# Kernel optimization log

Measured on AMD Instinct MI355X. Metric: run time of the kernel, lower is better.

The kernel has to match this reference:

```python
import jax, jax.numpy as jnp
import numpy as np

B, S, V, H, E, T, MAXLEN = 16, 100, 30000, 512, 300, 50, 50
NEG = -1e6


def setup_inputs() -> dict:
    key = jax.random.key(0)
    ks = jax.random.split(key, 12)
    D = 3 * H + E
    d = {}
    d["encoder_outputs"] = jax.random.normal(ks[0], (B, S, H), jnp.float32)
    d["temp_outputs"] = jax.random.normal(ks[1], (B, T, H), jnp.float32)
    d["z"] = jax.random.normal(ks[2], (B, H), jnp.float32)
    d["embedding"] = jax.random.normal(ks[3], (V, E), jnp.float32) * 0.02
    d["gru_w_ih"] = jax.random.normal(ks[4], (3 * H, D), jnp.float32) * (1.0 / np.sqrt(H))
    d["gru_w_hh"] = jax.random.normal(ks[5], (3 * H, H), jnp.float32) * (1.0 / np.sqrt(H))
    d["gru_b_ih"] = jnp.zeros((3 * H,), jnp.float32)
    d["gru_b_hh"] = jnp.zeros((3 * H,), jnp.float32)
    d["attn_w"] = jax.random.normal(ks[6], (H, H), jnp.float32) * (1.0 / np.sqrt(H))
    d["attn_b"] = jnp.zeros((H,), jnp.float32)
    d["copy_w"] = jax.random.normal(ks[7], (H, H), jnp.float32) * (1.0 / np.sqrt(H))
    d["copy_b"] = jnp.zeros((H,), jnp.float32)
    d["out_w"] = jax.random.normal(ks[8], (V, 2 * H), jnp.float32) * (1.0 / np.sqrt(2 * H))
    d["out_b"] = jnp.zeros((V,), jnp.float32)
    d["templates"] = jax.random.randint(ks[9], (B, T), 0, V, jnp.int32)
    d["inputs"] = jax.random.randint(ks[10], (B, S), 0, V, jnp.int32)
    return d


def _forward(encoder_outputs, temp_outputs, z, embedding,
             gru_w_ih, gru_w_hh, gru_b_ih, gru_b_hh,
             attn_w, attn_b, copy_w, copy_b, out_w, out_b,
             templates, inputs):
    # one-hot over extended vocab (vocab + source positions), as in to_one_hot
    one_hot = jax.nn.one_hot(inputs, V + S, dtype=jnp.float32)      # (B,S,V+S)
    missing = (one_hot.sum(axis=1) == 0).at[:, 0].set(True)          # (B,V+S)
    rows = jnp.arange(B)
    cols = jnp.arange(S)

    def gru_cell(x, h):  # torch nn.GRU single step
        gi = x @ gru_w_ih.T + gru_b_ih
        gh = h @ gru_w_hh.T + gru_b_hh
        ir, iz, inn = jnp.split(gi, 3, axis=-1)
        hr, hz, hn = jnp.split(gh, 3, axis=-1)
        r = jax.nn.sigmoid(ir + hr)
        zg = jax.nn.sigmoid(iz + hz)
        n = jnp.tanh(inn + r * hn)
        return (1.0 - zg) * n + zg * h

    def decode_step(prev_idx, pre_hidden, t_hidden, sel_read):
        idx = jnp.where(prev_idx > V, 3, prev_idx)                   # OOV -> <UNK>=3
        emb = embedding[idx]                                         # (B,E)
        x = jnp.concatenate([pre_hidden, t_hidden, sel_read, emb], axis=-1)
        hidden = gru_cell(x, pre_hidden)                             # (B,H); output==hidden for 1 step
        th = hidden @ attn_w.T + attn_b
        aw = jax.nn.softmax(jnp.einsum('bsh,bh->bs', encoder_outputs, th), axis=-1)
        context = jnp.einsum('bs,bsh->bh', aw, encoder_outputs)
        gen = jnp.concatenate([context, hidden], axis=-1) @ out_w.T + out_b
        gen = gen.at[:, 0].set(NEG)
        th2 = hidden @ copy_w.T + copy_b
        css = jnp.einsum('bsh,bh->bs', encoder_outputs, th2)         # copy_score_seq (B,S)
        copy_scores = jnp.where(missing, NEG, jnp.einsum('bs,bsv->bv', css, one_hot))
        probs = jax.nn.softmax(jnp.concatenate([gen, copy_scores], axis=-1), axis=-1)
        final = jnp.pad(probs[:, :V], ((0, 0), (0, S))) + probs[:, V:]  # (B,V+S)
        sampled = jnp.argmax(jnp.log(final + 1e-10), axis=-1).astype(jnp.int32)
        pos = one_hot[rows[:, None], cols[None, :], sampled[:, None]]   # (B,S)
        sel = pos * css
        sel = sel / jnp.maximum(jnp.sum(jnp.abs(sel), axis=-1, keepdims=True), 1e-12)
        new_sel = jnp.einsum('bs,bsh->bh', sel, encoder_outputs)
        return sampled, final, hidden, new_sel

    beg = jnp.ones((B,), jnp.int32)  # vocab['<BEG>'] == 1
    carry0 = dict(hidden=z, pre_hidden=z, sampled=beg, pre_sampled=beg, eos=beg,
                  pre_seg=templates[:, 0], index=jnp.zeros((B,), jnp.int32),
                  c_len=jnp.zeros((B,), jnp.int32), sel=jnp.zeros((B, H), jnp.float32))

    def body(c, _):
        # eos bookkeeping: keep last non-<EOS>(6) sample
        eos_new = jnp.where(c['pre_sampled'] == 6, c['eos'], c['pre_sampled'])
        # mask_tf=True template advance
        flag = (c['pre_seg'] != 5) | (c['pre_sampled'] == 6) | (c['c_len'] > 20)
        index = c['index'] + flag.astype(jnp.int32)
        c_len = c['c_len'] + (~flag).astype(jnp.int32)
        seg = templates[rows, index]
        t_hidden = temp_outputs[rows, index]                         # (B,H)
        sampled = jnp.where(flag, seg, c['sampled'])                 # masked_scatter of seg
        pre_sampled = sampled
        # rows emitting 5/6 keep their old pre_hidden
        keep = (sampled == 5) | (sampled == 6)
        pre_hidden = jnp.where(keep[:, None], c['pre_hidden'], c['hidden'])
        sampled = jnp.where(sampled == 6, eos_new, sampled)
        new_sampled, output, hidden, sel = decode_step(sampled, pre_hidden, t_hidden, c['sel'])
        new_c = dict(hidden=hidden, pre_hidden=pre_hidden, sampled=new_sampled,
                     pre_sampled=pre_sampled, eos=eos_new, pre_seg=seg,
                     index=index, c_len=c_len, sel=sel)
        return new_c, (output, pre_sampled)

    _, (outs, idxs) = jax.lax.scan(body, carry0, None, length=MAXLEN - 1)
    sos = jnp.zeros((B, V + S), jnp.float32).at[:, 1].set(1.0)
    decoder_outputs = jnp.concatenate([sos[:, None, :], jnp.swapaxes(outs, 0, 1)], axis=1)
    sampled_idxs = jnp.concatenate([beg[:, None], idxs.T], axis=1)
    return decoder_outputs, sampled_idxs


def reference(encoder_outputs, temp_outputs, z, embedding,
              gru_w_ih, gru_w_hh, gru_b_ih, gru_b_hh,
              attn_w, attn_b, copy_w, copy_b, out_w, out_b,
              templates, inputs):
    return _forward(encoder_outputs, temp_outputs, z, embedding,
                    gru_w_ih, gru_w_hh, gru_b_ih, gru_b_hh,
                    attn_w, attn_b, copy_w, copy_b, out_w, out_b,
                    templates, inputs)
```

## Files before the change

kernel.cpp:

```cpp
#include <hip/hip_runtime.h>
#include <math.h>

#define NEGV (-1000000.0f)

constexpr size_t WS_WT_OUT = 0;
constexpr size_t WS_WT_IH  = 30720000;
constexpr size_t WS_WT_HH  = 33540096;
constexpr size_t WS_WT_AT  = 34326528;
constexpr size_t WS_WT_CP  = 34588672;
constexpr size_t WS_XG     = 34850816;
constexpr size_t WS_X2     = 34880192;
constexpr size_t WS_PGI    = 34896576;
constexpr size_t WS_PGH    = 35093184;
constexpr size_t WS_PTH    = 35289792;
constexpr size_t WS_PTH2   = 35322560;
constexpr size_t WS_HID    = 35355328;
constexpr size_t WS_PREH   = 35363520;
constexpr size_t WS_CSS    = 35371712;
constexpr size_t WS_CVAL   = 35373312;
constexpr size_t WS_COPYZ  = 35374912;
constexpr size_t WS_MCUR   = 35374928;
constexpr size_t WS_ZPART  = 35374944;
constexpr size_t WS_ZTOT   = 35382480;
constexpr size_t WS_INTS   = 35383264;
constexpr size_t IP_CTOK = 0;
constexpr size_t IP_EOS  = 1600;
constexpr size_t IP_PS   = 1616;
constexpr size_t IP_SEG  = 1632;
constexpr size_t IP_IDX  = 1648;
constexpr size_t IP_CLEN = 1664;

constexpr size_t OUT_BSTRIDE = 1505000;
constexpr size_t IDX_OFF = 24080000;

__global__ void ktrans(const float* __restrict__ src, float* __restrict__ dst, int R, int C) {
  __shared__ float tile[32][33];
  const int t = threadIdx.x;
  const int lx = t & 31, ly = t >> 5;
  const int r0 = blockIdx.x * 32, c0 = blockIdx.y * 32;
  #pragma unroll
  for (int i = 0; i < 4; ++i) {
    int r = r0 + ly + i * 8, c = c0 + lx;
    if (r < R && c < C) tile[ly + i * 8][lx] = src[(size_t)r * C + c];
  }
  __syncthreads();
  #pragma unroll
  for (int i = 0; i < 4; ++i) {
    int c = c0 + ly + i * 8, r = r0 + lx;
    if (r < R && c < C) dst[(size_t)c * R + r] = tile[lx][ly + i * 8];
  }
}

__global__ void kinit(float* ws, float* out, const float* __restrict__ z,
                      const int* __restrict__ templates, const float* __restrict__ temp_outputs,
                      const float* __restrict__ embedding) {
  const int bid = blockIdx.x, t = threadIdx.x;
  if (bid < 1882) {
    int e = bid * 256 + t;
    if (e < 16 * 30100) {
      int b = e / 30100, v = e % 30100;
      out[(size_t)b * OUT_BSTRIDE + v] = (v == 1) ? 1.0f : 0.0f;
    }
    return;
  }
  const int b = bid - 1882;
  const int tpl0 = templates[b * 50];
  const int ps = 1, eos = 1;
  const int eos_new = (ps == 6) ? eos : ps;
  const bool flag = (tpl0 != 5) || (ps == 6);
  const int index = flag ? 1 : 0;
  const int clen = flag ? 0 : 1;
  const int seg = templates[b * 50 + index];
  const int sampled2 = flag ? seg : 1;
  const int sampled3 = (sampled2 == 6) ? eos_new : sampled2;
  const int idx_emb = (sampled3 > 30000) ? 3 : (sampled3 > 29999 ? 29999 : sampled3);
  float* xg = ws + WS_XG;
  for (int d = t; d < 512; d += 256) {
    float zv = z[b * 512 + d];
    xg[d * 16 + b] = zv;
    ws[WS_PREH + b * 512 + d] = zv;
    xg[(512 + d) * 16 + b] = temp_outputs[(size_t)(b * 50 + index) * 512 + d];
    xg[(1024 + d) * 16 + b] = 0.0f;
  }
  for (int d = t; d < 300; d += 256)
    xg[(1536 + d) * 16 + b] = embedding[(size_t)idx_emb * 300 + d];
  if (t == 0) {
    int* ip = (int*)ws;
    ip[WS_INTS + IP_EOS + b] = eos_new;
    ip[WS_INTS + IP_PS + b] = sampled2;
    ip[WS_INTS + IP_SEG + b] = seg;
    ip[WS_INTS + IP_IDX + b] = index;
    ip[WS_INTS + IP_CLEN + b] = clen;
    out[IDX_OFF + b * 50 + 0] = 1.0f;
    out[IDX_OFF + b * 50 + 1] = (float)sampled2;
  }
}

__global__ void k1(float* ws) {
  const int bid = blockIdx.x, t = threadIdx.x;
  const int lane = t & 63;
  const int bq = __builtin_amdgcn_readfirstlane(t >> 6);
  const int b0 = bq * 4;
  const float* xg = ws + WS_XG;
  const bool is_gi = bid < 192;
  const int sub = is_gi ? bid : bid - 192;
  const int jc = sub >> 3, ks = sub & 7;
  const int j = jc * 64 + lane;
  const float* W;
  int d0, d1;
  float* pout;
  if (is_gi) {
    W = ws + WS_WT_IH; d0 = ks * 230; d1 = d0 + 230; if (d1 > 1836) d1 = 1836;
    pout = ws + WS_PGI;
  } else {
    W = ws + WS_WT_HH; d0 = ks * 64; d1 = d0 + 64;
    pout = ws + WS_PGH;
  }
  float a0 = 0.f, a1 = 0.f, a2 = 0.f, a3 = 0.f;
  const float* xrow = xg + b0;
  for (int d = d0; d < d1; ++d) {
    float w = W[(size_t)d * 1536 + j];
    float4 xv = *(const float4*)(xrow + d * 16);
    a0 += w * xv.x; a1 += w * xv.y; a2 += w * xv.z; a3 += w * xv.w;
  }
  *(float4*)(pout + ((size_t)ks * 1536 + j) * 16 + b0) = make_float4(a0, a1, a2, a3);
}

__global__ void k1b(float* ws, const float* __restrict__ bih, const float* __restrict__ bhh) {
  const int bid = blockIdx.x;
  const int b = bid >> 1;
  const int j = (bid & 1) * 256 + threadIdx.x;
  float gir = 0.f, giz = 0.f, gin = 0.f, ghr = 0.f, ghz = 0.f, ghn = 0.f;
  #pragma unroll
  for (int ks = 0; ks < 8; ++ks) {
    const float* pg = ws + WS_PGI + (size_t)ks * 1536 * 16;
    gir += pg[j * 16 + b]; giz += pg[(512 + j) * 16 + b]; gin += pg[(1024 + j) * 16 + b];
    const float* ph = ws + WS_PGH + (size_t)ks * 1536 * 16;
    ghr += ph[j * 16 + b]; ghz += ph[(512 + j) * 16 + b]; ghn += ph[(1024 + j) * 16 + b];
  }
  gir += bih[j]; giz += bih[512 + j]; gin += bih[1024 + j];
  ghr += bhh[j]; ghz += bhh[512 + j]; ghn += bhh[1024 + j];
  float r  = 1.f / (1.f + expf(-(gir + ghr)));
  float zg = 1.f / (1.f + expf(-(giz + ghz)));
  float n  = tanhf(gin + r * ghn);
  float h  = ws[WS_PREH + b * 512 + j];
  float hn = (1.f - zg) * n + zg * h;
  ws[WS_HID + b * 512 + j] = hn;
  ws[WS_X2 + (size_t)(512 + j) * 16 + b] = hn;
}

__global__ void k2(float* ws) {
  const int bid = blockIdx.x, t = threadIdx.x;
  const int lane = t & 63;
  const int bq = __builtin_amdgcn_readfirstlane(t >> 6);
  const int b0 = bq * 4;
  const bool is_th = bid < 32;
  const int sub = is_th ? bid : bid - 32;
  const int jc = sub >> 2, ks = sub & 3;
  const int j = jc * 64 + lane;
  const float* W = ws + (is_th ? WS_WT_AT : WS_WT_CP);
  float* pout = ws + (is_th ? WS_PTH : WS_PTH2);
  const float* xh = ws + WS_X2 + 512 * 16 + b0;
  const int d0 = ks * 128, d1 = d0 + 128;
  float a0 = 0.f, a1 = 0.f, a2 = 0.f, a3 = 0.f;
  for (int d = d0; d < d1; ++d) {
    float w = W[(size_t)d * 512 + j];
    float4 xv = *(const float4*)(xh + d * 16);
    a0 += w * xv.x; a1 += w * xv.y; a2 += w * xv.z; a3 += w * xv.w;
  }
  *(float4*)(pout + ((size_t)ks * 512 + j) * 16 + b0) = make_float4(a0, a1, a2, a3);
}

__global__ void k2b(float* ws, const float* __restrict__ attn_b, const float* __restrict__ copy_b,
                    const float* __restrict__ enc, const int* __restrict__ inputs) {
  const int b = blockIdx.x, t = threadIdx.x;
  __shared__ float th_s[512], th2_s[512];
  __shared__ float sc_s[128], css_s[128], e_s[128];
  __shared__ float aw_s[100];
  __shared__ int   tok_s[100];
  __shared__ float gs_s[100];
  __shared__ int   valid_s[100];
  __shared__ float red[256];

  for (int j = t; j < 512; j += 256) {
    float s1 = attn_b[j], s2 = copy_b[j];
    #pragma unroll
    for (int ks = 0; ks < 4; ++ks) {
      s1 += ws[WS_PTH  + ((size_t)ks * 512 + j) * 16 + b];
      s2 += ws[WS_PTH2 + ((size_t)ks * 512 + j) * 16 + b];
    }
    th_s[j] = s1; th2_s[j] = s2;
  }
  if (t < 128) { sc_s[t] = -1e30f; css_s[t] = 0.f; }
  if (t < 100) tok_s[t] = inputs[b * 100 + t];
  __syncthreads();

  const int w = t >> 6, lane = t & 63;
  for (int s = w; s < 100; s += 4) {
    const float* er = enc + (size_t)(b * 100 + s) * 512;
    float p1 = 0.f, p2 = 0.f;
    #pragma unroll
    for (int i = 0; i < 8; ++i) {
      float e = er[lane + 64 * i];
      p1 += e * th_s[lane + 64 * i];
      p2 += e * th2_s[lane + 64 * i];
    }
    for (int off = 32; off > 0; off >>= 1) { p1 += __shfl_down(p1, off); p2 += __shfl_down(p2, off); }
    if (lane == 0) { sc_s[s] = p1; css_s[s] = p2; ws[WS_CSS + b * 100 + s] = p2; }
  }
  __syncthreads();

  if (t < 64) {
    float m = fmaxf(sc_s[t], sc_s[t + 64]);
    for (int off = 32; off > 0; off >>= 1) m = fmaxf(m, __shfl_down(m, off));
    if (t == 0) red[0] = m;
  }
  __syncthreads();
  const float m = red[0];
  if (t < 128) e_s[t] = (t < 100) ? expf(sc_s[t] - m) : 0.f;
  __syncthreads();
  if (t < 64) {
    float ss = e_s[t] + e_s[t + 64];
    for (int off = 32; off > 0; off >>= 1) ss += __shfl_down(ss, off);
    if (t == 0) red[1] = ss;
  }
  __syncthreads();
  const float inv = 1.f / red[1];
  if (t < 100) aw_s[t] = e_s[t] * inv;
  __syncthreads();

  for (int d = t; d < 512; d += 256) {
    float c = 0.f;
    for (int s = 0; s < 100; ++s) c += aw_s[s] * enc[(size_t)(b * 100 + s) * 512 + d];
    ws[WS_X2 + (size_t)d * 16 + b] = c;
  }

  if (t < 100) {
    int tok = tok_s[t]; float gs = 0.f; bool first = true;
    for (int s2 = 0; s2 < 100; ++s2) {
      if (tok_s[s2] == tok) { gs += css_s[s2]; if (s2 < t) first = false; }
    }
    gs_s[t] = gs; valid_s[t] = (first && tok != 0) ? 1 : 0;
  }
  __syncthreads();
  if (t < 64) {
    float v1 = (t < 100 && valid_s[t]) ? gs_s[t] : -1e30f;
    float v2 = ((t + 64) < 100 && valid_s[t + 64]) ? gs_s[t + 64] : -1e30f;
    float m2 = fmaxf(v1, v2);
    for (int off = 32; off > 0; off >>= 1) m2 = fmaxf(m2, __shfl_down(m2, off));
    if (t == 0) red[2] = fmaxf(m2, 0.f);
  }
  __syncthreads();
  const float M = red[2];
  float cv = 0.f;
  if (t < 100) {
    cv = valid_s[t] ? expf(gs_s[t] - M) : 0.f;
    ws[WS_CVAL + b * 100 + t] = cv;
    ((int*)ws)[WS_INTS + IP_CTOK + b * 100 + t] = tok_s[t];
  }
  red[t] = cv;
  __syncthreads();
  for (int off = 128; off > 0; off >>= 1) { if (t < off) red[t] += red[t + off]; __syncthreads(); }
  if (t == 0) { ws[WS_COPYZ + b] = red[0]; ws[WS_MCUR + b] = M; }
}

__global__ void k3(float* ws, const float* __restrict__ outb, float* out, int step) {
  const int bid = blockIdx.x, t = threadIdx.x;
  const int lane = t & 63;
  const int bq = __builtin_amdgcn_readfirstlane(t >> 6);
  const int b0 = bq * 4;
  const int v = bid * 64 + lane;
  const float* Wt = ws + WS_WT_OUT;
  const float* xrow = ws + WS_X2 + b0;
  float p0 = 0.f, p1 = 0.f, p2 = 0.f, p3 = 0.f;
  if (v < 30000) {
    float a0 = 0.f, a1 = 0.f, a2 = 0.f, a3 = 0.f;
    #pragma unroll 8
    for (int k = 0; k < 1024; ++k) {
      float wv = Wt[(size_t)k * 30000 + v];
      float4 xv = *(const float4*)(xrow + k * 16);
      a0 += wv * xv.x; a1 += wv * xv.y; a2 += wv * xv.z; a3 += wv * xv.w;
    }
    if (v != 0) {
      const float bb = outb[v];
      p0 = expf(a0 + bb - ws[WS_MCUR + b0 + 0]);
      p1 = expf(a1 + bb - ws[WS_MCUR + b0 + 1]);
      p2 = expf(a2 + bb - ws[WS_MCUR + b0 + 2]);
      p3 = expf(a3 + bb - ws[WS_MCUR + b0 + 3]);
    }
  }
  if (v < 30100) {
    const size_t rb = (size_t)(step + 1) * 30100 + v;
    out[(size_t)(b0 + 0) * OUT_BSTRIDE + rb] = p0;
    out[(size_t)(b0 + 1) * OUT_BSTRIDE + rb] = p1;
    out[(size_t)(b0 + 2) * OUT_BSTRIDE + rb] = p2;
    out[(size_t)(b0 + 3) * OUT_BSTRIDE + rb] = p3;
  }
  float s0 = p0, s1 = p1, s2 = p2, s3 = p3;
  for (int off = 32; off > 0; off >>= 1) {
    s0 += __shfl_down(s0, off); s1 += __shfl_down(s1, off);
    s2 += __shfl_down(s2, off); s3 += __shfl_down(s3, off);
  }
  __shared__ float wp[4][4];
  if (lane == 0) { wp[bq][0] = s0; wp[bq][1] = s1; wp[bq][2] = s2; wp[bq][3] = s3; }
  __syncthreads();
  if (t < 16) ws[WS_ZPART + (size_t)bid * 16 + t] = wp[t >> 2][t & 3];
}

__global__ void k4b(float* ws, float* out, const float* __restrict__ enc, const int* __restrict__ inputs,
                    const int* __restrict__ templates, const float* __restrict__ temp_outputs,
                    const float* __restrict__ embedding, int step) {
  const int b = blockIdx.x, t = threadIdx.x;
  int* ip = (int*)ws;
  const size_t row = (size_t)b * OUT_BSTRIDE + (size_t)(step + 1) * 30100;
  __shared__ float red[256];
  __shared__ int redi[256];
  __shared__ float selv_s[100];
  __shared__ float sh_inv;

  float zp = 0.f;
  for (int i = t; i < 471; i += 256) zp += ws[WS_ZPART + (size_t)i * 16 + b];
  red[t] = zp; __syncthreads();
  for (int off = 128; off > 0; off >>= 1) { if (t < off) red[t] += red[t + off]; __syncthreads(); }
  if (t == 0) ws[WS_ZTOT + step * 16 + b] = red[0] + ws[WS_COPYZ + b];
  __syncthreads();

  if (t < 100) {
    float cv = ws[WS_CVAL + b * 100 + t];
    if (cv > 0.f) {
      int tok = ip[WS_INTS + IP_CTOK + b * 100 + t];
      out[row + tok] += cv;
    }
  }
  __syncthreads();
  if (step >= 48) return;

  float bp = -1.f; int bv = 0;
  for (int v = t; v < 30100; v += 256) {
    float p = out[row + v];
    if (p > bp) { bp = p; bv = v; }
  }
  red[t] = bp; redi[t] = bv; __syncthreads();
  for (int off = 128; off > 0; off >>= 1) {
    if (t < off) {
      float po = red[t + off]; int vo = redi[t + off];
      if (po > red[t] || (po == red[t] && vo < redi[t])) { red[t] = po; redi[t] = vo; }
    }
    __syncthreads();
  }
  const int samp = redi[0];
  __syncthreads();

  float sv = 0.f;
  if (t < 100) {
    sv = (inputs[b * 100 + t] == samp) ? ws[WS_CSS + b * 100 + t] : 0.f;
    selv_s[t] = sv;
  }
  red[t] = (t < 100) ? fabsf(sv) : 0.f;
  __syncthreads();
  for (int off = 128; off > 0; off >>= 1) { if (t < off) red[t] += red[t + off]; __syncthreads(); }
  if (t == 0) sh_inv = 1.f / fmaxf(red[0], 1e-12f);
  __syncthreads();
  if (t < 100) selv_s[t] = selv_s[t] * sh_inv;
  __syncthreads();

  const int ps = ip[WS_INTS + IP_PS + b], eos = ip[WS_INTS + IP_EOS + b];
  const int preseg = ip[WS_INTS + IP_SEG + b], index = ip[WS_INTS + IP_IDX + b];
  const int clen = ip[WS_INTS + IP_CLEN + b];
  const int eos_new = (ps == 6) ? eos : ps;
  const bool flag = (preseg != 5) || (ps == 6) || (clen > 20);
  const int index_n = index + (flag ? 1 : 0);
  const int clen_n = clen + (flag ? 0 : 1);
  const int seg = templates[b * 50 + index_n];
  const int sampled2 = flag ? seg : samp;
  const bool keep = (sampled2 == 5) || (sampled2 == 6);
  const int sampled3 = (sampled2 == 6) ? eos_new : sampled2;
  const int idx_emb = (sampled3 > 30000) ? 3 : (sampled3 > 29999 ? 29999 : sampled3);

  float* xg = ws + WS_XG;
  for (int d = t; d < 512; d += 256) {
    float phv = keep ? ws[WS_PREH + b * 512 + d] : ws[WS_HID + b * 512 + d];
    ws[WS_PREH + b * 512 + d] = phv;
    xg[d * 16 + b] = phv;
    xg[(512 + d) * 16 + b] = temp_outputs[(size_t)(b * 50 + index_n) * 512 + d];
    float sr = 0.f;
    for (int s = 0; s < 100; ++s) sr += selv_s[s] * enc[(size_t)(b * 100 + s) * 512 + d];
    xg[(1024 + d) * 16 + b] = sr;
  }
  for (int d = t; d < 300; d += 256)
    xg[(1536 + d) * 16 + b] = embedding[(size_t)idx_emb * 300 + d];
  if (t == 0) {
    ip[WS_INTS + IP_PS + b] = sampled2;
    ip[WS_INTS + IP_EOS + b] = eos_new;
    ip[WS_INTS + IP_SEG + b] = seg;
    ip[WS_INTS + IP_IDX + b] = index_n;
    ip[WS_INTS + IP_CLEN + b] = clen_n;
    out[IDX_OFF + b * 50 + step + 2] = (float)sampled2;
  }
}

__global__ void knorm(const float* __restrict__ ws, float* out) {
  const int e = blockIdx.x * 256 + threadIdx.x;
  if (e >= 23598400) return;
  const int b = e / 1474900;
  const int r2 = e - b * 1474900;
  const int r = r2 / 30100;
  const int v = r2 - r * 30100;
  out[(size_t)b * OUT_BSTRIDE + (size_t)(r + 1) * 30100 + v] /= ws[WS_ZTOT + r * 16 + b];
}

extern "C" void kernel_launch(void* const* d_in, const int* in_sizes, int n_in,
                              void* d_out, int out_size, void* d_ws, size_t ws_size,
                              hipStream_t stream) {
  const float* enc       = (const float*)d_in[0];
  const float* temp_out  = (const float*)d_in[1];
  const float* z         = (const float*)d_in[2];
  const float* embedding = (const float*)d_in[3];
  const float* gru_w_ih  = (const float*)d_in[4];
  const float* gru_w_hh  = (const float*)d_in[5];
  const float* gru_b_ih  = (const float*)d_in[6];
  const float* gru_b_hh  = (const float*)d_in[7];
  const float* attn_w    = (const float*)d_in[8];
  const float* attn_b    = (const float*)d_in[9];
  const float* copy_w    = (const float*)d_in[10];
  const float* copy_b    = (const float*)d_in[11];
  const float* out_w     = (const float*)d_in[12];
  const float* out_b     = (const float*)d_in[13];
  const int*   templates = (const int*)d_in[14];
  const int*   inputs    = (const int*)d_in[15];
  float* out = (float*)d_out;
  float* ws  = (float*)d_ws;

  ktrans<<<dim3(938, 32), 256, 0, stream>>>(out_w, ws + WS_WT_OUT, 30000, 1024);
  ktrans<<<dim3(48, 58), 256, 0, stream>>>(gru_w_ih, ws + WS_WT_IH, 1536, 1836);
  ktrans<<<dim3(48, 16), 256, 0, stream>>>(gru_w_hh, ws + WS_WT_HH, 1536, 512);
  ktrans<<<dim3(16, 16), 256, 0, stream>>>(attn_w, ws + WS_WT_AT, 512, 512);
  ktrans<<<dim3(16, 16), 256, 0, stream>>>(copy_w, ws + WS_WT_CP, 512, 512);

  kinit<<<1898, 256, 0, stream>>>(ws, out, z, templates, temp_out, embedding);

  for (int step = 0; step < 49; ++step) {
    k1<<<384, 256, 0, stream>>>(ws);
    k1b<<<32, 256, 0, stream>>>(ws, gru_b_ih, gru_b_hh);
    k2<<<64, 256, 0, stream>>>(ws);
    k2b<<<16, 256, 0, stream>>>(ws, attn_b, copy_b, enc, inputs);
    k3<<<471, 256, 0, stream>>>(ws, out_b, out, step);
    k4b<<<16, 256, 0, stream>>>(ws, out, enc, inputs, templates, temp_out, embedding, step);
  }

  knorm<<<92182, 256, 0, stream>>>(ws, out);
}
```

Measured before the change: 11.62 ms.

## Store output projection weights in bf16 and fuse argmax into logits kernel

The transposed 30000x1024 output weight matrix is stored as bf16 instead of fp32, halving the bytes k3 streams on each of the 49 decode steps. k3 also computes a per-block argmax of its logits and writes it to workspace. k4b then reduces these partial maxima and checks only the copy-token positions, instead of rescanning the full 30100-wide output row. bf16 weights add rounding error that could flip greedy argmax picks relative to the fp32 reference.

```diff
diff --git a/kernel.cpp b/kernel.cpp
--- a/kernel.cpp
+++ b/kernel.cpp
@@ -4,34 +4,42 @@
 #define NEGV (-1000000.0f)
 
 constexpr size_t WS_WT_OUT = 0;
-constexpr size_t WS_WT_IH  = 30720000;
-constexpr size_t WS_WT_HH  = 33540096;
-constexpr size_t WS_WT_AT  = 34326528;
-constexpr size_t WS_WT_CP  = 34588672;
-constexpr size_t WS_XG     = 34850816;
-constexpr size_t WS_X2     = 34880192;
-constexpr size_t WS_PGI    = 34896576;
-constexpr size_t WS_PGH    = 35093184;
-constexpr size_t WS_PTH    = 35289792;
-constexpr size_t WS_PTH2   = 35322560;
-constexpr size_t WS_HID    = 35355328;
-constexpr size_t WS_PREH   = 35363520;
-constexpr size_t WS_CSS    = 35371712;
-constexpr size_t WS_CVAL   = 35373312;
-constexpr size_t WS_COPYZ  = 35374912;
-constexpr size_t WS_MCUR   = 35374928;
-constexpr size_t WS_ZPART  = 35374944;
-constexpr size_t WS_ZTOT   = 35382480;
-constexpr size_t WS_INTS   = 35383264;
+constexpr size_t WS_WT_IH  = 15360000;
+constexpr size_t WS_WT_HH  = 18180096;
+constexpr size_t WS_WT_AT  = 18966528;
+constexpr size_t WS_WT_CP  = 19228672;
+constexpr size_t WS_XG     = 19490816;
+constexpr size_t WS_X2     = 19520192;
+constexpr size_t WS_PGI    = 19536576;
+constexpr size_t WS_PGH    = 19733184;
+constexpr size_t WS_PTH    = 19929792;
+constexpr size_t WS_PTH2   = 19962560;
+constexpr size_t WS_HID    = 19995328;
+constexpr size_t WS_PREH   = 20003520;
+constexpr size_t WS_CSS    = 20011712;
+constexpr size_t WS_CVAL   = 20013312;
+constexpr size_t WS_COPYZ  = 20014912;
+constexpr size_t WS_MCUR   = 20014928;
+constexpr size_t WS_ZPART  = 20014944;
+constexpr size_t WS_ZTOT   = 20022480;
+constexpr size_t WS_AMV    = 20023264;
+constexpr size_t WS_INTS   = 20030800;
 constexpr size_t IP_CTOK = 0;
 constexpr size_t IP_EOS  = 1600;
 constexpr size_t IP_PS   = 1616;
 constexpr size_t IP_SEG  = 1632;
 constexpr size_t IP_IDX  = 1648;
 constexpr size_t IP_CLEN = 1664;
+constexpr size_t IP_AMI  = 1680;
 
 constexpr size_t OUT_BSTRIDE = 1505000;
 constexpr size_t IDX_OFF = 24080000;
+
+__device__ inline unsigned short f2bf(float x) {
+  unsigned u = __float_as_uint(x);
+  unsigned r = (u + 0x7fffu + ((u >> 16) & 1u)) >> 16;
+  return (unsigned short)r;
+}
 
 __global__ void ktrans(const float* __restrict__ src, float* __restrict__ dst, int R, int C) {
   __shared__ float tile[32][33];
@@ -48,6 +56,24 @@
   for (int i = 0; i < 4; ++i) {
     int c = c0 + ly + i * 8, r = r0 + lx;
     if (r < R && c < C) dst[(size_t)c * R + r] = tile[lx][ly + i * 8];
+  }
+}
+
+__global__ void ktransb(const float* __restrict__ src, unsigned short* __restrict__ dst, int R, int C) {
+  __shared__ float tile[32][33];
+  const int t = threadIdx.x;
+  const int lx = t & 31, ly = t >> 5;
+  const int r0 = blockIdx.x * 32, c0 = blockIdx.y * 32;
+  #pragma unroll
+  for (int i = 0; i < 4; ++i) {
+    int r = r0 + ly + i * 8, c = c0 + lx;
+    if (r < R && c < C) tile[ly + i * 8][lx] = src[(size_t)r * C + c];
+  }
+  __syncthreads();
+  #pragma unroll
+  for (int i = 0; i < 4; ++i) {
+    int c = c0 + ly + i * 8, r = r0 + lx;
+    if (r < R && c < C) dst[(size_t)c * R + r] = f2bf(tile[lx][ly + i * 8]);
   }
 }
 
@@ -96,7 +122,7 @@
   }
 }
 
-__global__ void k1(float* ws) {
+__global__ __launch_bounds__(256) void k1(float* ws) {
   const int bid = blockIdx.x, t = threadIdx.x;
   const int lane = t & 63;
   const int bq = __builtin_amdgcn_readfirstlane(t >> 6);
@@ -126,7 +152,7 @@
   *(float4*)(pout + ((size_t)ks * 1536 + j) * 16 + b0) = make_float4(a0, a1, a2, a3);
 }
 
-__global__ void k1b(float* ws, const float* __restrict__ bih, const float* __restrict__ bhh) {
+__global__ __launch_bounds__(256) void k1b(float* ws, const float* __restrict__ bih, const float* __restrict__ bhh) {
   const int bid = blockIdx.x;
   const int b = bid >> 1;
   const int j = (bid & 1) * 256 + threadIdx.x;
@@ -149,7 +175,7 @@
   ws[WS_X2 + (size_t)(512 + j) * 16 + b] = hn;
 }
 
-__global__ void k2(float* ws) {
+__global__ __launch_bounds__(256) void k2(float* ws) {
   const int bid = blockIdx.x, t = threadIdx.x;
   const int lane = t & 63;
   const int bq = __builtin_amdgcn_readfirstlane(t >> 6);
@@ -171,7 +197,7 @@
   *(float4*)(pout + ((size_t)ks * 512 + j) * 16 + b0) = make_float4(a0, a1, a2, a3);
 }
 
-__global__ void k2b(float* ws, const float* __restrict__ attn_b, const float* __restrict__ copy_b,
+__global__ __launch_bounds__(256) void k2b(float* ws, const float* __restrict__ attn_b, const float* __restrict__ copy_b,
                     const float* __restrict__ enc, const int* __restrict__ inputs) {
   const int b = blockIdx.x, t = threadIdx.x;
   __shared__ float th_s[512], th2_s[512];
@@ -264,20 +290,21 @@
   if (t == 0) { ws[WS_COPYZ + b] = red[0]; ws[WS_MCUR + b] = M; }
 }
 
-__global__ void k3(float* ws, const float* __restrict__ outb, float* out, int step) {
+__global__ __launch_bounds__(256) void k3(float* ws, const float* __restrict__ outb, float* out, int step) {
   const int bid = blockIdx.x, t = threadIdx.x;
   const int lane = t & 63;
   const int bq = __builtin_amdgcn_readfirstlane(t >> 6);
   const int b0 = bq * 4;
   const int v = bid * 64 + lane;
-  const float* Wt = ws + WS_WT_OUT;
+  const unsigned short* Wt = (const unsigned short*)(ws + WS_WT_OUT);
   const float* xrow = ws + WS_X2 + b0;
   float p0 = 0.f, p1 = 0.f, p2 = 0.f, p3 = 0.f;
   if (v < 30000) {
     float a0 = 0.f, a1 = 0.f, a2 = 0.f, a3 = 0.f;
-    #pragma unroll 8
+    #pragma unroll 16
     for (int k = 0; k < 1024; ++k) {
-      float wv = Wt[(size_t)k * 30000 + v];
+      unsigned short wu = Wt[(size_t)k * 30000 + v];
+      float wv = __uint_as_float(((unsigned)wu) << 16);
       float4 xv = *(const float4*)(xrow + k * 16);
       a0 += wv * xv.x; a1 += wv * xv.y; a2 += wv * xv.z; a3 += wv * xv.w;
     }
@@ -301,13 +328,28 @@
     s0 += __shfl_down(s0, off); s1 += __shfl_down(s1, off);
     s2 += __shfl_down(s2, off); s3 += __shfl_down(s3, off);
   }
+  float m0 = p0, m1 = p1, m2 = p2, m3 = p3;
+  int i0 = v, i1 = v, i2 = v, i3 = v;
+  for (int off = 32; off > 0; off >>= 1) {
+    float q; int qi;
+    q = __shfl_down(m0, off); qi = __shfl_down(i0, off); if (q > m0 || (q == m0 && qi < i0)) { m0 = q; i0 = qi; }
+    q = __shfl_down(m1, off); qi = __shfl_down(i1, off); if (q > m1 || (q == m1 && qi < i1)) { m1 = q; i1 = qi; }
+    q = __shfl_down(m2, off); qi = __shfl_down(i2, off); if (q > m2 || (q == m2 && qi < i2)) { m2 = q; i2 = qi; }
+    q = __shfl_down(m3, off); qi = __shfl_down(i3, off); if (q > m3 || (q == m3 && qi < i3)) { m3 = q; i3 = qi; }
+  }
   __shared__ float wp[4][4];
-  if (lane == 0) { wp[bq][0] = s0; wp[bq][1] = s1; wp[bq][2] = s2; wp[bq][3] = s3; }
+  if (lane == 0) {
+    wp[bq][0] = s0; wp[bq][1] = s1; wp[bq][2] = s2; wp[bq][3] = s3;
+    float* amv = ws + WS_AMV + (size_t)bid * 16 + b0;
+    int* ami = ((int*)ws) + WS_INTS + IP_AMI + (size_t)bid * 16 + b0;
+    amv[0] = m0; amv[1] = m1; amv[2] = m2; amv[3] = m3;
+    ami[0] = i0; ami[1] = i1; ami[2] = i2; ami[3] = i3;
+  }
   __syncthreads();
   if (t < 16) ws[WS_ZPART + (size_t)bid * 16 + t] = wp[t >> 2][t & 3];
 }
 
-__global__ void k4b(float* ws, float* out, const float* __restrict__ enc, const int* __restrict__ inputs,
+__global__ __launch_bounds__(256) void k4b(float* ws, float* out, const float* __restrict__ enc, const int* __restrict__ inputs,
                     const int* __restrict__ templates, const float* __restrict__ temp_outputs,
                     const float* __restrict__ embedding, int step) {
   const int b = blockIdx.x, t = threadIdx.x;
@@ -317,29 +359,20 @@
   __shared__ int redi[256];
   __shared__ float selv_s[100];
   __shared__ float sh_inv;
+  __shared__ float gbv_s; __shared__ int gbi_s;
 
   float zp = 0.f;
-  for (int i = t; i < 471; i += 256) zp += ws[WS_ZPART + (size_t)i * 16 + b];
+  float bp = -1.f; int bv = 0x7fffffff;
+  for (int i = t; i < 471; i += 256) {
+    zp += ws[WS_ZPART + (size_t)i * 16 + b];
+    float av = ws[WS_AMV + (size_t)i * 16 + b];
+    int ai = ip[WS_INTS + IP_AMI + (size_t)i * 16 + b];
+    if (av > bp || (av == bp && ai < bv)) { bp = av; bv = ai; }
+  }
   red[t] = zp; __syncthreads();
   for (int off = 128; off > 0; off >>= 1) { if (t < off) red[t] += red[t + off]; __syncthreads(); }
   if (t == 0) ws[WS_ZTOT + step * 16 + b] = red[0] + ws[WS_COPYZ + b];
   __syncthreads();
-
-  if (t < 100) {
-    float cv = ws[WS_CVAL + b * 100 + t];
-    if (cv > 0.f) {
-      int tok = ip[WS_INTS + IP_CTOK + b * 100 + t];
-      out[row + tok] += cv;
-    }
-  }
-  __syncthreads();
-  if (step >= 48) return;
-
-  float bp = -1.f; int bv = 0;
-  for (int v = t; v < 30100; v += 256) {
-    float p = out[row + v];
-    if (p > bp) { bp = p; bv = v; }
-  }
   red[t] = bp; redi[t] = bv; __syncthreads();
   for (int off = 128; off > 0; off >>= 1) {
     if (t < off) {
@@ -348,7 +381,34 @@
     }
     __syncthreads();
   }
-  const int samp = redi[0];
+  if (t == 0) { gbv_s = red[0]; gbi_s = redi[0]; }
+  __syncthreads();
+
+  float cv = 0.f; int tok = 0;
+  if (t < 100) {
+    cv = ws[WS_CVAL + b * 100 + t];
+    tok = ip[WS_INTS + IP_CTOK + b * 100 + t];
+    if (cv > 0.f) out[row + tok] += cv;
+  }
+  __syncthreads();
+  if (step >= 48) return;
+
+  float sv_ = -1.f; int si_ = 0x7fffffff;
+  if (t < 100 && cv > 0.f) { sv_ = out[row + tok]; si_ = tok; }
+  red[t] = sv_; redi[t] = si_; __syncthreads();
+  for (int off = 128; off > 0; off >>= 1) {
+    if (t < off) {
+      float po = red[t + off]; int vo = redi[t + off];
+      if (po > red[t] || (po == red[t] && vo < redi[t])) { red[t] = po; redi[t] = vo; }
+    }
+    __syncthreads();
+  }
+  int samp;
+  {
+    float sbv = red[0]; int sbi = redi[0];
+    float gv = gbv_s; int gi = gbi_s;
+    samp = (sbv > gv || (sbv == gv && sbi < gi)) ? sbi : gi;
+  }
   __syncthreads();
 
   float sv = 0.f;
@@ -431,7 +491,7 @@
   float* out = (float*)d_out;
   float* ws  = (float*)d_ws;
 
-  ktrans<<<dim3(938, 32), 256, 0, stream>>>(out_w, ws + WS_WT_OUT, 30000, 1024);
+  ktransb<<<dim3(938, 32), 256, 0, stream>>>(out_w, (unsigned short*)(ws + WS_WT_OUT), 30000, 1024);
   ktrans<<<dim3(48, 58), 256, 0, stream>>>(gru_w_ih, ws + WS_WT_IH, 1536, 1836);
   ktrans<<<dim3(48, 16), 256, 0, stream>>>(gru_w_hh, ws + WS_WT_HH, 1536, 512);
   ktrans<<<dim3(16, 16), 256, 0, stream>>>(attn_w, ws + WS_WT_AT, 512, 512);
```

New measurement: 9.790 ms. -15.7%, faster.
